# Performance work log

Hardware: AMD Instinct MI355X
Metric: run time of the kernel (lower is better)

Reference implementation:

```python
import jax, jax.numpy as jnp
import numpy as np

N = 50000
E = 800000
IN_C = 128
HID = 64
HEADS = 2
OUT_C = 40
NEG_SLOPE = 0.2


def glorot(key, shape):
    fan_in, fan_out = shape[0], shape[-1]
    lim = jnp.sqrt(6.0 / (fan_in + fan_out))
    return jax.random.uniform(key, shape, jnp.float32, -lim, lim)


def setup_inputs() -> dict:
    key = jax.random.key(0)
    ks = jax.random.split(key, 10)
    x = jax.random.normal(ks[0], (N, IN_C), jnp.float32)
    edge_index = jax.random.randint(ks[1], (2, E), 0, N, jnp.int32)
    # layer 1: heads=2, concat -> out features HEADS*HID
    W1 = glorot(ks[2], (IN_C, HEADS * HID))
    att_src1 = glorot(ks[3], (HEADS, HID))
    att_dst1 = glorot(ks[4], (HEADS, HID))
    b1 = jnp.zeros((HEADS * HID,), jnp.float32)
    # layer 2: out_heads=1, concat=False (mean over the single head)
    W2 = glorot(ks[5], (HEADS * HID, 1 * OUT_C))
    att_src2 = glorot(ks[6], (1, OUT_C))
    att_dst2 = glorot(ks[7], (1, OUT_C))
    b2 = jnp.zeros((OUT_C,), jnp.float32)
    return {"x": x, "edge_index": edge_index,
            "W1": W1, "att_src1": att_src1, "att_dst1": att_dst1, "b1": b1,
            "W2": W2, "att_src2": att_src2, "att_dst2": att_dst2, "b2": b2}


def _segment_softmax(logits, seg, num_segments):
    # logits: [E, H]; softmax over edges sharing the same destination node
    m = jax.ops.segment_max(logits, seg, num_segments=num_segments)
    m = jnp.where(jnp.isfinite(m), m, 0.0)
    e = jnp.exp(logits - m[seg])
    s = jax.ops.segment_sum(e, seg, num_segments=num_segments)
    return e / (s[seg] + 1e-16)


def _gat_conv(x, src, dst, W, a_src, a_dst, b, concat, n_nodes):
    H, C = a_src.shape
    h = (x @ W).reshape(n_nodes, H, C)                    # [N, H, C]
    al_src = jnp.einsum('nhc,hc->nh', h, a_src)           # [N, H]
    al_dst = jnp.einsum('nhc,hc->nh', h, a_dst)           # [N, H]
    e = jax.nn.leaky_relu(al_src[src] + al_dst[dst], NEG_SLOPE)  # [E, H]
    alpha = _segment_softmax(e, dst, n_nodes)             # [E, H]
    msg = h[src] * alpha[:, :, None]                      # [E, H, C]
    out = jax.ops.segment_sum(msg, dst, num_segments=n_nodes)
    out = out.reshape(n_nodes, H * C) if concat else out.mean(axis=1)
    return out + b


def reference(x, edge_index, W1, att_src1, att_dst1, b1, W2, att_src2, att_dst2, b2):
    n_nodes = x.shape[0]
    loop = jnp.arange(n_nodes, dtype=edge_index.dtype)
    src = jnp.concatenate([edge_index[0], loop])  # add self loops
    dst = jnp.concatenate([edge_index[1], loop])
    # eval mode: dropout is identity, use_bn=False -> no batchnorm
    h = _gat_conv(x, src, dst, W1, att_src1, att_dst1, b1, True, n_nodes)
    h = jax.nn.elu(h)
    out = _gat_conv(h, src, dst, W2, att_src2, att_dst2, b2, False, n_nodes)
    return out
```

## Files before the change

kernel.cpp:

```cpp
#include <hip/hip_runtime.h>
#include <hip/hip_fp16.h>

#define NEG_SLOPE 0.2f

typedef _Float16 f16x8 __attribute__((ext_vector_type(8)));
typedef float f32x4 __attribute__((ext_vector_type(4)));

__device__ __forceinline__ int h2i(__half2 h) { return *(int*)&h; }
__device__ __forceinline__ __half2 i2h(int i) { return *(__half2*)&i; }
__device__ __forceinline__ float lrelu(float v) { return (v > 0.f) ? v : NEG_SLOPE * v; }
__device__ __forceinline__ int pkmax(int a, int b) {
    int r;
    asm("v_pk_max_f16 %0, %1, %2" : "=v"(r) : "v"(a), "v"(b));
    return r;
}
__device__ __forceinline__ __half selh(int r, int packed) {
    return (r < 8) ? __low2half(i2h(packed)) : __high2half(i2h(packed));
}

union U16x8 { uint4 u; __half2 h[4]; };
union U16x4 { uint2 u; __half2 h[2]; };

__global__ __launch_bounds__(256) void k_pack(const float* __restrict__ W1,
                                              const float* __restrict__ W2,
                                              _Float16* __restrict__ bp1,
                                              _Float16* __restrict__ bp2,
                                              int* __restrict__ cnt, int N) {
    int idx = blockIdx.x * 256 + threadIdx.x;
    if (idx < N) cnt[idx] = 0;
    if (idx < 16384) {
        int j = idx & 7, l = (idx >> 3) & 63, nt = (idx >> 9) & 7, ks = idx >> 12;
        int k = ks * 32 + (l >> 4) * 8 + j;
        int col = nt * 16 + (l & 15);
        bp1[idx] = (_Float16)W1[k * 128 + col];
    }
    int idx2 = idx - 16384;
    if (idx2 >= 0 && idx2 < 6144) {
        int j = idx2 & 7, l = (idx2 >> 3) & 63, q = idx2 >> 9;
        int nt = q % 3, ks = q / 3;
        int k = ks * 32 + (l >> 4) * 8 + j;
        int col = nt * 16 + (l & 15);
        bp2[idx2] = (col < 40) ? (_Float16)W2[k * 40 + col] : (_Float16)0.f;
    }
}

__global__ __launch_bounds__(256) void k_bg(
    const int* __restrict__ ei, int* __restrict__ cnt,
    unsigned short* __restrict__ colell, int E, int ps, int gB,
    const float* __restrict__ x, const _Float16* __restrict__ bp1,
    const float* __restrict__ as1, const float* __restrict__ ad1,
    __half2* __restrict__ h1h, float* __restrict__ alsrc, float* __restrict__ aldst,
    int N) {
    if (blockIdx.x < gB) {
        int p = blockIdx.x & 7;
        int e = ((blockIdx.x >> 3) * blockDim.x + threadIdx.x) * 2;
        if (e >= E) return;
        int lo = p * ps, hi = lo + ps;
        int2 d2 = *(const int2*)(ei + E + e);
        if (d2.x >= lo && d2.x < hi) {
            int s = ei[e];
            int rank = atomicAdd(&cnt[d2.x], 1);
            if (rank < 64) colell[(size_t)d2.x * 64 + rank] = (unsigned short)s;
        }
        if (e + 1 < E && d2.y >= lo && d2.y < hi) {
            int s = ei[e + 1];
            int rank = atomicAdd(&cnt[d2.y], 1);
            if (rank < 64) colell[(size_t)d2.y * 64 + rank] = (unsigned short)s;
        }
        return;
    }
    int bid = blockIdx.x - gB;
    int w = threadIdx.x >> 6, l = threadIdx.x & 63;
    int n0 = bid * 64 + w * 16;
    int li = l & 15, lg = l >> 4;
    int arow = n0 + li;
    f16x8 a[4];
#pragma unroll
    for (int ks = 0; ks < 4; ks++) {
        float4 p0 = make_float4(0, 0, 0, 0), p1 = make_float4(0, 0, 0, 0);
        if (arow < N) {
            const float4* src = (const float4*)(x + (size_t)arow * 128 + ks * 32 + lg * 8);
            p0 = src[0];
            p1 = src[1];
        }
        f16x8 t;
        t[0] = (_Float16)p0.x; t[1] = (_Float16)p0.y; t[2] = (_Float16)p0.z; t[3] = (_Float16)p0.w;
        t[4] = (_Float16)p1.x; t[5] = (_Float16)p1.y; t[6] = (_Float16)p1.z; t[7] = (_Float16)p1.w;
        a[ks] = t;
    }
    f32x4 acc[8];
#pragma unroll
    for (int nt = 0; nt < 8; nt++) acc[nt] = (f32x4){0.f, 0.f, 0.f, 0.f};
    const f16x8* bp = (const f16x8*)bp1;
#pragma unroll
    for (int nt = 0; nt < 8; nt++)
#pragma unroll
        for (int ks = 0; ks < 4; ks++)
            acc[nt] = __builtin_amdgcn_mfma_f32_16x16x32_f16(a[ks], bp[(ks * 8 + nt) * 64 + l],
                                                             acc[nt], 0, 0, 0);
    float as1v[8], ad1v[8];
#pragma unroll
    for (int nt = 0; nt < 8; nt++) {
        as1v[nt] = as1[nt * 16 + li];
        ad1v[nt] = ad1[nt * 16 + li];
    }
#pragma unroll
    for (int r = 0; r < 4; r++) {
        float ps0 = 0, ps1 = 0, pd0 = 0, pd1 = 0;
#pragma unroll
        for (int nt = 0; nt < 4; nt++) {
            ps0 = fmaf(acc[nt][r], as1v[nt], ps0);
            pd0 = fmaf(acc[nt][r], ad1v[nt], pd0);
        }
#pragma unroll
        for (int nt = 4; nt < 8; nt++) {
            ps1 = fmaf(acc[nt][r], as1v[nt], ps1);
            pd1 = fmaf(acc[nt][r], ad1v[nt], pd1);
        }
#pragma unroll
        for (int o = 1; o < 16; o <<= 1) {
            ps0 += __shfl_xor(ps0, o);
            ps1 += __shfl_xor(ps1, o);
            pd0 += __shfl_xor(pd0, o);
            pd1 += __shfl_xor(pd1, o);
        }
        int node = n0 + lg * 4 + r;
        if (li == 0 && node < N) {
            alsrc[node * 2] = ps0;
            alsrc[node * 2 + 1] = ps1;
            aldst[node * 2] = pd0;
            aldst[node * 2 + 1] = pd1;
        }
    }
#pragma unroll
    for (int nt = 0; nt < 8; nt++)
#pragma unroll
        for (int r = 0; r < 4; r++) {
            float v = acc[nt][r];
            float p = __shfl_down(v, 1);
            int node = n0 + lg * 4 + r;
            if ((l & 1) == 0 && node < N)
                h1h[(size_t)node * 64 + nt * 8 + (li >> 1)] = __floats2half2_rn(v, p);
        }
}

__global__ __launch_bounds__(256) void k_gemm2(
    const _Float16* __restrict__ hf, const _Float16* __restrict__ bp2,
    const float* __restrict__ as2, const float* __restrict__ ad2,
    __half2* __restrict__ h2h, float* __restrict__ alsrc, float* __restrict__ aldst,
    int N) {
    int w = threadIdx.x >> 6, l = threadIdx.x & 63;
    int n0 = blockIdx.x * 64 + w * 16;
    int li = l & 15, lg = l >> 4;
    int arow = n0 + li;
    const f16x8* hfv = (const f16x8*)hf;
    f16x8 a[4];
#pragma unroll
    for (int ks = 0; ks < 4; ks++) {
        f16x8 t;
        if (arow < N) {
            t = hfv[(size_t)arow * 16 + ks * 4 + lg];
        } else {
#pragma unroll
            for (int k = 0; k < 8; k++) t[k] = (_Float16)0.f;
        }
        a[ks] = t;
    }
    f32x4 acc[3];
#pragma unroll
    for (int nt = 0; nt < 3; nt++) acc[nt] = (f32x4){0.f, 0.f, 0.f, 0.f};
    const f16x8* bp = (const f16x8*)bp2;
#pragma unroll
    for (int nt = 0; nt < 3; nt++)
#pragma unroll
        for (int ks = 0; ks < 4; ks++)
            acc[nt] = __builtin_amdgcn_mfma_f32_16x16x32_f16(a[ks], bp[(ks * 3 + nt) * 64 + l],
                                                             acc[nt], 0, 0, 0);
    float as2v[3], ad2v[3];
#pragma unroll
    for (int nt = 0; nt < 3; nt++) {
        int col = nt * 16 + li;
        as2v[nt] = (col < 40) ? as2[col] : 0.f;
        ad2v[nt] = (col < 40) ? ad2[col] : 0.f;
    }
#pragma unroll
    for (int r = 0; r < 4; r++) {
        float ps = 0, pd = 0;
#pragma unroll
        for (int nt = 0; nt < 3; nt++) {
            ps = fmaf(acc[nt][r], as2v[nt], ps);
            pd = fmaf(acc[nt][r], ad2v[nt], pd);
        }
#pragma unroll
        for (int o = 1; o < 16; o <<= 1) {
            ps += __shfl_xor(ps, o);
            pd += __shfl_xor(pd, o);
        }
        int node = n0 + lg * 4 + r;
        if (li == 0 && node < N) {
            alsrc[node] = ps;
            aldst[node] = pd;
        }
    }
#pragma unroll
    for (int nt = 0; nt < 3; nt++)
#pragma unroll
        for (int r = 0; r < 4; r++) {
            float v = acc[nt][r];
            float p = __shfl_down(v, 1);
            int node = n0 + lg * 4 + r;
            int col = nt * 16 + li;
            if ((l & 1) == 0 && col < 40 && node < N)
                h2h[(size_t)node * 20 + nt * 8 + (li >> 1)] = __floats2half2_rn(v, p);
        }
}

__global__ __launch_bounds__(256) void k_gather1(
    const int* __restrict__ cnt, const unsigned short* __restrict__ colell,
    const _Float16* __restrict__ h1, const float2* __restrict__ alsrc,
    const float2* __restrict__ aldst, const float4* __restrict__ b1v,
    _Float16* __restrict__ hf, int N) {
    int wave = (int)(((size_t)blockIdx.x * blockDim.x + threadIdx.x) >> 6);
    int lane = threadIdx.x & 63;
    int h = lane >> 5, hl = lane & 31, h32 = h << 5;
    int wid = wave * 2 + h;
    bool valid = wid < N;
    int widc = valid ? wid : 0;
    int g = hl >> 4, r = hl & 15;
    float2 asn = alsrc[widc], ad = aldst[widc];
    float ls0 = valid ? lrelu(asn.x + ad.x) : 0.f;
    float ls1 = valid ? lrelu(asn.y + ad.y) : 0.f;
    int nb = valid ? min(cnt[wid], 64) : 0;
    int nbmax = max(nb, __shfl_xor(nb, 32));
    bool big = nbmax > 32;
    int sva = 0;
    float l0a = -1e30f, l1a = -1e30f;
    if (hl < nb) {
        sva = colell[(size_t)wid * 64 + hl];
        float2 av = alsrc[sva];
        l0a = lrelu(av.x + ad.x);
        l1a = lrelu(av.y + ad.y);
    }
    int svb = 0, web = 0;
    float l0b = -1e30f, l1b = -1e30f;
    if (big && hl + 32 < nb) {
        svb = colell[(size_t)wid * 64 + 32 + hl];
        float2 av = alsrc[svb];
        l0b = lrelu(av.x + ad.x);
        l1b = lrelu(av.y + ad.y);
    }
    int lpi = h2i(__floats2half2_rn(l0a, l1a));
    if (big) lpi = pkmax(lpi, h2i(__floats2half2_rn(l0b, l1b)));
#pragma unroll
    for (int o = 16; o > 0; o >>= 1) lpi = pkmax(lpi, __shfl_xor(lpi, o));
    __half2 lp = i2h(lpi);
    float m0 = fmaxf(__low2float(lp), ls0);
    float m1 = fmaxf(__high2float(lp), ls1);
    float e0a = (hl < nb) ? __expf(l0a - m0) : 0.f;
    float e1a = (hl < nb) ? __expf(l1a - m1) : 0.f;
    int wea = h2i(__floats2half2_rn(e0a, e1a));
    if (big) {
        float e0b = (hl + 32 < nb) ? __expf(l0b - m0) : 0.f;
        float e1b = (hl + 32 < nb) ? __expf(l1b - m1) : 0.f;
        web = h2i(__floats2half2_rn(e0b, e1b));
    }
    float lsh = (r < 8) ? ls0 : ls1;
    float mh = (r < 8) ? m0 : m1;
    __half esh = __float2half((g == 0) ? __expf(lsh - mh) : 0.f);
    float s_part = __half2float(esh);
    __half2 esp = __half2half2(esh);
    U16x8 hs;
    hs.u = *(const uint4*)(h1 + (size_t)widc * 128 + r * 8);
    __half2 a0 = __hmul2(hs.h[0], esp), a1 = __hmul2(hs.h[1], esp),
            a2 = __hmul2(hs.h[2], esp), a3 = __hmul2(hs.h[3], esp);
    int i0 = __shfl(sva, h32 + g),     p0 = __shfl(wea, h32 + g);
    int i1 = __shfl(sva, h32 + 2 + g), p1 = __shfl(wea, h32 + 2 + g);
    int i2 = __shfl(sva, h32 + 4 + g), p2 = __shfl(wea, h32 + 4 + g);
    int i3 = __shfl(sva, h32 + 6 + g), p3 = __shfl(wea, h32 + 6 + g);
    U16x8 hA, hB, hC, hD;
    hA.u = *(const uint4*)(h1 + (size_t)i0 * 128 + r * 8);
    hB.u = *(const uint4*)(h1 + (size_t)i1 * 128 + r * 8);
    hC.u = *(const uint4*)(h1 + (size_t)i2 * 128 + r * 8);
    hD.u = *(const uint4*)(h1 + (size_t)i3 * 128 + r * 8);
    __half wA = selh(r, p0), wB = selh(r, p1), wC = selh(r, p2), wD = selh(r, p3);
    for (int j = 8; j < nbmax; j += 2) {
        int slot = j + g;
        int i4, p4;
        if (j < 32) {
            i4 = __shfl(sva, h32 + slot);
            p4 = __shfl(wea, h32 + slot);
        } else {
            i4 = __shfl(svb, h32 + slot - 32);
            p4 = __shfl(web, h32 + slot - 32);
        }
        U16x8 hN;
        hN.u = *(const uint4*)(h1 + (size_t)i4 * 128 + r * 8);
        __half2 ww = __half2half2(wA);
        s_part += __half2float(wA);
        a0 = __hfma2(ww, hA.h[0], a0);
        a1 = __hfma2(ww, hA.h[1], a1);
        a2 = __hfma2(ww, hA.h[2], a2);
        a3 = __hfma2(ww, hA.h[3], a3);
        hA = hB; wA = wB;
        hB = hC; wB = wC;
        hC = hD; wC = wD;
        hD = hN; wD = selh(r, p4);
    }
    {
        __half2 ww = __half2half2(wA);
        s_part += __half2float(wA);
        a0 = __hfma2(ww, hA.h[0], a0); a1 = __hfma2(ww, hA.h[1], a1);
        a2 = __hfma2(ww, hA.h[2], a2); a3 = __hfma2(ww, hA.h[3], a3);
    }
    {
        __half2 ww = __half2half2(wB);
        s_part += __half2float(wB);
        a0 = __hfma2(ww, hB.h[0], a0); a1 = __hfma2(ww, hB.h[1], a1);
        a2 = __hfma2(ww, hB.h[2], a2); a3 = __hfma2(ww, hB.h[3], a3);
    }
    {
        __half2 ww = __half2half2(wC);
        s_part += __half2float(wC);
        a0 = __hfma2(ww, hC.h[0], a0); a1 = __hfma2(ww, hC.h[1], a1);
        a2 = __hfma2(ww, hC.h[2], a2); a3 = __hfma2(ww, hC.h[3], a3);
    }
    {
        __half2 ww = __half2half2(wD);
        s_part += __half2float(wD);
        a0 = __hfma2(ww, hD.h[0], a0); a1 = __hfma2(ww, hD.h[1], a1);
        a2 = __hfma2(ww, hD.h[2], a2); a3 = __hfma2(ww, hD.h[3], a3);
    }
    s_part += __shfl_xor(s_part, 16);
    a0 = __hadd2(a0, i2h(__shfl_xor(h2i(a0), 16)));
    a1 = __hadd2(a1, i2h(__shfl_xor(h2i(a1), 16)));
    a2 = __hadd2(a2, i2h(__shfl_xor(h2i(a2), 16)));
    a3 = __hadd2(a3, i2h(__shfl_xor(h2i(a3), 16)));
    if (g == 0 && valid) {
        float inv = 1.f / (s_part + 1e-16f);
        float4 bA = b1v[2 * r], bB = b1v[2 * r + 1];
        float v[8] = {__low2float(a0), __high2float(a0), __low2float(a1), __high2float(a1),
                      __low2float(a2), __high2float(a2), __low2float(a3), __high2float(a3)};
        float vb[8] = {bA.x, bA.y, bA.z, bA.w, bB.x, bB.y, bB.z, bB.w};
        U16x8 o;
#pragma unroll
        for (int k = 0; k < 8; k += 2) {
            float u0 = fmaf(v[k], inv, vb[k]);
            float u1 = fmaf(v[k + 1], inv, vb[k + 1]);
            u0 = (u0 > 0.f) ? u0 : (__expf(u0) - 1.f);
            u1 = (u1 > 0.f) ? u1 : (__expf(u1) - 1.f);
            o.h[k >> 1] = __floats2half2_rn(u0, u1);
        }
        *(uint4*)(hf + (size_t)wid * 128 + r * 8) = o.u;
    }
}

__global__ __launch_bounds__(256) void k_gather2(
    const int* __restrict__ cnt, const unsigned short* __restrict__ colell,
    const _Float16* __restrict__ h2, const float* __restrict__ alsrc,
    const float* __restrict__ aldst, const float4* __restrict__ b2v,
    float4* __restrict__ out4, int N) {
    int wave = (int)(((size_t)blockIdx.x * blockDim.x + threadIdx.x) >> 6);
    int lane = threadIdx.x & 63;
    int h = lane >> 5, hl = lane & 31, h32 = h << 5;
    int wid = wave * 2 + h;
    bool valid = wid < N;
    int widc = valid ? wid : 0;
    int g = hl >> 4, r = hl & 15;
    int rc = (r < 10) ? r : 0;
    float ad = valid ? aldst[wid] : 0.f;
    float ls = valid ? lrelu(alsrc[wid] + ad) : 0.f;
    int nb = valid ? min(cnt[wid], 64) : 0;
    int nbmax = max(nb, __shfl_xor(nb, 32));
    bool big = nbmax > 32;
    int sva = 0;
    float la = -1e30f;
    if (hl < nb) {
        sva = colell[(size_t)wid * 64 + hl];
        la = lrelu(alsrc[sva] + ad);
    }
    int svb = 0;
    float lb = -1e30f, eb = 0.f;
    if (big && hl + 32 < nb) {
        svb = colell[(size_t)wid * 64 + 32 + hl];
        lb = lrelu(alsrc[svb] + ad);
    }
    float m = fmaxf(la, lb);
#pragma unroll
    for (int o = 16; o > 0; o >>= 1) m = fmaxf(m, __shfl_xor(m, o));
    m = fmaxf(m, ls);
    float ea = (hl < nb) ? __expf(la - m) : 0.f;
    if (big) eb = (hl + 32 < nb) ? __expf(lb - m) : 0.f;
    float es = (g == 0) ? __expf(ls - m) : 0.f;
    float s_part = es;
    __half2 esp = __floats2half2_rn(es, es);
    U16x4 hs;
    hs.u = *(const uint2*)(h2 + (size_t)widc * 40 + rc * 4);
    __half2 a0 = __hmul2(hs.h[0], esp), a1 = __hmul2(hs.h[1], esp);
    int i0 = __shfl(sva, h32 + g);
    int i1 = __shfl(sva, h32 + 2 + g);
    int i2 = __shfl(sva, h32 + 4 + g);
    int i3 = __shfl(sva, h32 + 6 + g);
    float wA = __shfl(ea, h32 + g), wB = __shfl(ea, h32 + 2 + g);
    float wC = __shfl(ea, h32 + 4 + g), wD = __shfl(ea, h32 + 6 + g);
    U16x4 hA, hB, hC, hD;
    hA.u = *(const uint2*)(h2 + (size_t)i0 * 40 + rc * 4);
    hB.u = *(const uint2*)(h2 + (size_t)i1 * 40 + rc * 4);
    hC.u = *(const uint2*)(h2 + (size_t)i2 * 40 + rc * 4);
    hD.u = *(const uint2*)(h2 + (size_t)i3 * 40 + rc * 4);
    for (int j = 8; j < nbmax; j += 2) {
        int slot = j + g;
        int i4;
        float wN;
        if (j < 32) {
            i4 = __shfl(sva, h32 + slot);
            wN = __shfl(ea, h32 + slot);
        } else {
            i4 = __shfl(svb, h32 + slot - 32);
            wN = __shfl(eb, h32 + slot - 32);
        }
        U16x4 hN;
        hN.u = *(const uint2*)(h2 + (size_t)i4 * 40 + rc * 4);
        __half2 ww = __floats2half2_rn(wA, wA);
        s_part += wA;
        a0 = __hfma2(ww, hA.h[0], a0);
        a1 = __hfma2(ww, hA.h[1], a1);
        hA = hB; wA = wB;
        hB = hC; wB = wC;
        hC = hD; wC = wD;
        hD = hN; wD = wN;
    }
    {
        __half2 ww = __floats2half2_rn(wA, wA);
        s_part += wA;
        a0 = __hfma2(ww, hA.h[0], a0); a1 = __hfma2(ww, hA.h[1], a1);
    }
    {
        __half2 ww = __floats2half2_rn(wB, wB);
        s_part += wB;
        a0 = __hfma2(ww, hB.h[0], a0); a1 = __hfma2(ww, hB.h[1], a1);
    }
    {
        __half2 ww = __floats2half2_rn(wC, wC);
        s_part += wC;
        a0 = __hfma2(ww, hC.h[0], a0); a1 = __hfma2(ww, hC.h[1], a1);
    }
    {
        __half2 ww = __floats2half2_rn(wD, wD);
        s_part += wD;
        a0 = __hfma2(ww, hD.h[0], a0); a1 = __hfma2(ww, hD.h[1], a1);
    }
    s_part += __shfl_xor(s_part, 16);
    a0 = __hadd2(a0, i2h(__shfl_xor(h2i(a0), 16)));
    a1 = __hadd2(a1, i2h(__shfl_xor(h2i(a1), 16)));
    if (g == 0 && r < 10 && valid) {
        float inv = 1.f / (s_part + 1e-16f);
        float4 b = b2v[r];
        float4 o = make_float4(fmaf(__low2float(a0), inv, b.x),
                               fmaf(__high2float(a0), inv, b.y),
                               fmaf(__low2float(a1), inv, b.z),
                               fmaf(__high2float(a1), inv, b.w));
        out4[(size_t)wid * 10 + r] = o;
    }
}

extern "C" void kernel_launch(void* const* d_in, const int* in_sizes, int n_in,
                              void* d_out, int out_size, void* d_ws, size_t ws_size,
                              hipStream_t stream) {
    const float* x   = (const float*)d_in[0];
    const int*   ei  = (const int*)d_in[1];
    const float* W1  = (const float*)d_in[2];
    const float* as1 = (const float*)d_in[3];
    const float* ad1 = (const float*)d_in[4];
    const float* b1  = (const float*)d_in[5];
    const float* W2  = (const float*)d_in[6];
    const float* as2 = (const float*)d_in[7];
    const float* ad2 = (const float*)d_in[8];
    const float* b2  = (const float*)d_in[9];
    int N = in_sizes[0] / 128;
    int E = in_sizes[1] / 2;
    float4* out4 = (float4*)d_out;

    char* ws = (char*)d_ws;
    size_t off = 0;
    auto alloc = [&](size_t bytes) {
        char* p = ws + off;
        off += (bytes + 255) & ~(size_t)255;
        return p;
    };
    int*            cnt    = (int*)alloc((size_t)N * 4);
    unsigned short* colell = (unsigned short*)alloc((size_t)N * 64 * 2);
    _Float16*       bp1    = (_Float16*)alloc(16384 * 2);
    _Float16*       bp2    = (_Float16*)alloc(6144 * 2);
    _Float16*       h1h    = (_Float16*)alloc((size_t)N * 128 * 2);
    _Float16*       hf     = (_Float16*)alloc((size_t)N * 128 * 2);
    _Float16*       h2h    = (_Float16*)alloc((size_t)N * 40 * 2);
    float*          alsrc1 = (float*)alloc((size_t)N * 2 * 4);
    float*          aldst1 = (float*)alloc((size_t)N * 2 * 4);
    float*          alsrc2 = (float*)alloc((size_t)N * 4);
    float*          aldst2 = (float*)alloc((size_t)N * 4);

    dim3 b256(256);
    int ps = (N + 7) / 8;
    int gB = 8 * ((E + 511) / 512);
    int gG = (N + 63) / 64;
    int gP = (N > 22528 ? N + 255 : 22528 + 255) / 256;

    k_pack<<<gP, b256, 0, stream>>>(W1, W2, bp1, bp2, cnt, N);
    k_bg<<<gB + gG, b256, 0, stream>>>(ei, cnt, colell, E, ps, gB,
                                       x, bp1, as1, ad1, (__half2*)h1h, alsrc1, aldst1, N);

    int nwaves = (N + 1) / 2;
    int gGa = (nwaves + 3) / 4;
    k_gather1<<<gGa, b256, 0, stream>>>(
        cnt, colell, h1h, (const float2*)alsrc1, (const float2*)aldst1,
        (const float4*)b1, hf, N);
    k_gemm2<<<gG, b256, 0, stream>>>(hf, bp2, as2, ad2, (__half2*)h2h, alsrc2, aldst2, N);
    k_gather2<<<gGa, b256, 0, stream>>>(
        cnt, colell, h2h, alsrc2, aldst2, (const float4*)b2, out4, N);
}
```

Measured before the change: 123.4 us.

## Bucket edges by destination block before building ELL in shared memory

Replaces the 8-pass global-atomic ELL build with a two-stage scheme. A partition kernel bins edges into 128-node buckets using shared-memory histograms and packed (dst,src) words. Each bucket block then builds its ELL rows in LDS with local atomics and writes them out coalesced. This removes the repeated full edge scans and the scattered global atomics, but adds a kernel launch and assumes a fixed bucket capacity (BCAP=3072), which can overflow on skewed degree distributions.

```diff
diff --git a/kernel.cpp b/kernel.cpp
--- a/kernel.cpp
+++ b/kernel.cpp
@@ -2,6 +2,7 @@
 #include <hip/hip_fp16.h>
 
 #define NEG_SLOPE 0.2f
+#define BCAP 3072
 
 typedef _Float16 f16x8 __attribute__((ext_vector_type(8)));
 typedef float f32x4 __attribute__((ext_vector_type(4)));
@@ -25,9 +26,9 @@
                                               const float* __restrict__ W2,
                                               _Float16* __restrict__ bp1,
                                               _Float16* __restrict__ bp2,
-                                              int* __restrict__ cnt, int N) {
+                                              int* __restrict__ top, int nbk) {
     int idx = blockIdx.x * 256 + threadIdx.x;
-    if (idx < N) cnt[idx] = 0;
+    if (idx < nbk) top[idx] = idx * BCAP;
     if (idx < 16384) {
         int j = idx & 7, l = (idx >> 3) & 63, nt = (idx >> 9) & 7, ks = idx >> 12;
         int k = ks * 32 + (l >> 4) * 8 + j;
@@ -44,33 +45,75 @@
     }
 }
 
+__global__ __launch_bounds__(256) void k_part(const int* __restrict__ ei,
+                                              int* __restrict__ top,
+                                              unsigned* __restrict__ part,
+                                              int E, int nbk) {
+    __shared__ int hist[400];
+    __shared__ int cbase[400];
+    int tid = threadIdx.x;
+    int e0 = blockIdx.x * 4096;
+    for (int i = tid; i < nbk; i += 256) hist[i] = 0;
+    __syncthreads();
+    unsigned word[16];
+    int brk[16];
+#pragma unroll
+    for (int k = 0; k < 16; k++) {
+        int e = e0 + k * 256 + tid;
+        brk[k] = -1;
+        if (e < E) {
+            int d = ei[E + e];
+            int s = ei[e];
+            int b = d >> 7;
+            int r = atomicAdd(&hist[b], 1);
+            word[k] = ((unsigned)d << 16) | (unsigned)s;
+            brk[k] = (b << 13) | r;
+        }
+    }
+    __syncthreads();
+    for (int i = tid; i < nbk; i += 256) cbase[i] = atomicAdd(&top[i], hist[i]);
+    __syncthreads();
+#pragma unroll
+    for (int k = 0; k < 16; k++) {
+        if (brk[k] >= 0) {
+            int b = brk[k] >> 13, r = brk[k] & 8191;
+            part[cbase[b] + r] = word[k];
+        }
+    }
+}
+
 __global__ __launch_bounds__(256) void k_bg(
-    const int* __restrict__ ei, int* __restrict__ cnt,
-    unsigned short* __restrict__ colell, int E, int ps, int gB,
+    const unsigned* __restrict__ part, const int* __restrict__ top,
+    int* __restrict__ cnt, unsigned short* __restrict__ colell, int nbk,
     const float* __restrict__ x, const _Float16* __restrict__ bp1,
     const float* __restrict__ as1, const float* __restrict__ ad1,
     __half2* __restrict__ h1h, float* __restrict__ alsrc, float* __restrict__ aldst,
     int N) {
-    if (blockIdx.x < gB) {
-        int p = blockIdx.x & 7;
-        int e = ((blockIdx.x >> 3) * blockDim.x + threadIdx.x) * 2;
-        if (e >= E) return;
-        int lo = p * ps, hi = lo + ps;
-        int2 d2 = *(const int2*)(ei + E + e);
-        if (d2.x >= lo && d2.x < hi) {
-            int s = ei[e];
-            int rank = atomicAdd(&cnt[d2.x], 1);
-            if (rank < 64) colell[(size_t)d2.x * 64 + rank] = (unsigned short)s;
-        }
-        if (e + 1 < E && d2.y >= lo && d2.y < hi) {
-            int s = ei[e + 1];
-            int rank = atomicAdd(&cnt[d2.y], 1);
-            if (rank < 64) colell[(size_t)d2.y * 64 + rank] = (unsigned short)s;
-        }
+    __shared__ unsigned short ell[128 * 64];
+    __shared__ int lcnt[128];
+    int tid = threadIdx.x;
+    if (blockIdx.x < (unsigned)nbk) {
+        int bb = blockIdx.x;
+        int nodebase = bb << 7;
+        int cb = bb * BCAP;
+        int count = top[bb] - cb;
+        if (tid < 128) lcnt[tid] = 0;
+        __syncthreads();
+        for (int i = tid; i < count; i += 256) {
+            unsigned u = part[cb + i];
+            int dl = (int)(u >> 16) - nodebase;
+            int r = atomicAdd(&lcnt[dl], 1);
+            if (r < 64) ell[dl * 64 + r] = (unsigned short)(u & 0xFFFFu);
+        }
+        __syncthreads();
+        uint4* dst = (uint4*)(colell + (size_t)nodebase * 64);
+        const uint4* src = (const uint4*)ell;
+        for (int i = tid; i < 1024; i += 256) dst[i] = src[i];
+        if (tid < 128) cnt[nodebase + tid] = lcnt[tid];
         return;
     }
-    int bid = blockIdx.x - gB;
-    int w = threadIdx.x >> 6, l = threadIdx.x & 63;
+    int bid = blockIdx.x - nbk;
+    int w = tid >> 6, l = tid & 63;
     int n0 = bid * 64 + w * 16;
     int li = l & 15, lg = l >> 4;
     int arow = n0 + li;
@@ -480,6 +523,9 @@
     int E = in_sizes[1] / 2;
     float4* out4 = (float4*)d_out;
 
+    int nbk = (N + 127) >> 7;
+    int npad = nbk << 7;
+
     char* ws = (char*)d_ws;
     size_t off = 0;
     auto alloc = [&](size_t bytes) {
@@ -487,8 +533,10 @@
         off += (bytes + 255) & ~(size_t)255;
         return p;
     };
-    int*            cnt    = (int*)alloc((size_t)N * 4);
-    unsigned short* colell = (unsigned short*)alloc((size_t)N * 64 * 2);
+    int*            top    = (int*)alloc((size_t)nbk * 4);
+    unsigned*       part   = (unsigned*)alloc((size_t)nbk * BCAP * 4);
+    int*            cnt    = (int*)alloc((size_t)npad * 4);
+    unsigned short* colell = (unsigned short*)alloc((size_t)npad * 64 * 2);
     _Float16*       bp1    = (_Float16*)alloc(16384 * 2);
     _Float16*       bp2    = (_Float16*)alloc(6144 * 2);
     _Float16*       h1h    = (_Float16*)alloc((size_t)N * 128 * 2);
@@ -500,14 +548,14 @@
     float*          aldst2 = (float*)alloc((size_t)N * 4);
 
     dim3 b256(256);
-    int ps = (N + 7) / 8;
-    int gB = 8 * ((E + 511) / 512);
     int gG = (N + 63) / 64;
-    int gP = (N > 22528 ? N + 255 : 22528 + 255) / 256;
-
-    k_pack<<<gP, b256, 0, stream>>>(W1, W2, bp1, bp2, cnt, N);
-    k_bg<<<gB + gG, b256, 0, stream>>>(ei, cnt, colell, E, ps, gB,
-                                       x, bp1, as1, ad1, (__half2*)h1h, alsrc1, aldst1, N);
+    int gPart = (E + 4095) / 4096;
+    int gP = (22528 + 255) / 256;
+
+    k_pack<<<gP, b256, 0, stream>>>(W1, W2, bp1, bp2, top, nbk);
+    k_part<<<gPart, b256, 0, stream>>>(ei, top, part, E, nbk);
+    k_bg<<<nbk + gG, b256, 0, stream>>>(part, top, cnt, colell, nbk,
+                                        x, bp1, as1, ad1, (__half2*)h1h, alsrc1, aldst1, N);
 
     int nwaves = (N + 1) / 2;
     int gGa = (nwaves + 3) / 4;
```

After: 103.5 us. -16.1%, faster.
